# Kernel optimization log

Hardware: AMD Instinct MI355X
Metric: run time of the kernel (lower is better)

Reference implementation:

```python
import jax, jax.numpy as jnp
import numpy as np

N_NODES = 100_000
N_EDGES = 1_600_000
D_IN = 128
D_HID = 128
D_OUT = 128
N_GRAPHS = 1024


def setup_inputs() -> dict:
    key = jax.random.key(0)
    ks = jax.random.split(key, 7)
    x = jax.random.normal(ks[0], (N_NODES, D_IN), dtype=jnp.float32)
    edge_index = jax.random.randint(ks[1], (2, N_EDGES), 0, N_NODES, dtype=jnp.int32)
    batch = jnp.sort(jax.random.randint(ks[2], (N_NODES,), 0, N_GRAPHS, dtype=jnp.int32))
    W1 = jax.random.normal(ks[3], (D_IN, D_HID), dtype=jnp.float32) * (1.0 / np.sqrt(D_IN))
    b1 = jax.random.normal(ks[4], (D_HID,), dtype=jnp.float32) * 0.01
    W2 = jax.random.normal(ks[5], (D_HID, D_OUT), dtype=jnp.float32) * (1.0 / np.sqrt(D_HID))
    b2 = jax.random.normal(ks[6], (D_OUT,), dtype=jnp.float32) * 0.01
    return {"x": x, "edge_index": edge_index, "batch": batch,
            "W1": W1, "b1": b1, "W2": W2, "b2": b2, "num_graphs": N_GRAPHS}


def gcn_conv(x, edge_index, W, b):
    """PyG GCNConv: add self-loops, symmetric deg^{-1/2} norm, linear, scatter-add."""
    n = x.shape[0]
    xw = x @ W  # [N, H] -- transform before propagate, as PyG does
    loop = jnp.arange(n, dtype=edge_index.dtype)
    src = jnp.concatenate([edge_index[0], loop])  # message source (x_j)
    dst = jnp.concatenate([edge_index[1], loop])  # aggregation target
    deg = jax.ops.segment_sum(jnp.ones_like(dst, dtype=xw.dtype), dst, num_segments=n)
    dinv = jnp.where(deg > 0, jax.lax.rsqrt(deg), 0.0)
    norm = dinv[src] * dinv[dst]  # [E+N]
    out = jax.ops.segment_sum(norm[:, None] * xw[src], dst, num_segments=n)
    return out + b


def reference(x, edge_index, batch, W1, b1, W2, b2, num_graphs):
    h = jax.nn.relu(gcn_conv(x, edge_index, W1, b1))
    h = gcn_conv(h, edge_index, W2, b2)
    # global_mean_pool over graph ids
    s = jax.ops.segment_sum(h, batch, num_segments=num_graphs)          # [G, D_OUT]
    cnt = jax.ops.segment_sum(jnp.ones((x.shape[0],), h.dtype), batch, num_segments=num_graphs)
    return s / jnp.maximum(cnt, 1.0)[:, None]
```

## Files before the change

### kernel.cpp

```cpp
#include <hip/hip_runtime.h>

constexpr int D = 128;
constexpr int PAD = 48;
constexpr int EBLK = 4096;
constexpr int WNODE = 256;
constexpr int CAPW = 32;
constexpr int SCAP = 8192;

typedef __attribute__((ext_vector_type(8))) short short8;
typedef __attribute__((ext_vector_type(4))) float floatx4;
typedef __attribute__((ext_vector_type(2))) float floatx2;
typedef unsigned short ushort_t;
typedef unsigned char uchar_t;

static inline size_t ws_align(size_t x) { return (x + 255) & ~size_t(255); }

__device__ inline unsigned pack_bf16(float a, float b) {
  unsigned ua = __float_as_uint(a), ub = __float_as_uint(b);
  ua += 0x7fffu + ((ua >> 16) & 1u);
  ub += 0x7fffu + ((ub >> 16) & 1u);
  return ((ua >> 16) & 0xffffu) | (ub & 0xffff0000u);
}
__device__ inline ushort_t f32_to_bf16u(float f) {
  unsigned u = __float_as_uint(f);
  u += 0x7fffu + ((u >> 16) & 1u);
  return (ushort_t)(u >> 16);
}
__device__ inline float bf16u_to_f32(ushort_t u) {
  return __uint_as_float(((unsigned)u) << 16);
}
__device__ inline uchar_t f32_to_fp8(float v) {
  int p = __builtin_amdgcn_cvt_pk_fp8_f32(v, v, 0, false);
  return (uchar_t)(p & 0xff);
}
__device__ inline void fp8x4_acc(unsigned u, float* v) {
  floatx2 a = __builtin_amdgcn_cvt_pk_f32_fp8((int)u, false);
  floatx2 b = __builtin_amdgcn_cvt_pk_f32_fp8((int)u, true);
  v[0] += a.x; v[1] += a.y; v[2] += b.x; v[3] += b.y;
}
__device__ inline void fp8x4_acc2(unsigned u, floatx2* v) {
  v[0] += __builtin_amdgcn_cvt_pk_f32_fp8((int)u, false);
  v[1] += __builtin_amdgcn_cvt_pk_f32_fp8((int)u, true);
}

__global__ __launch_bounds__(256) void k_prep(
    const int* __restrict__ src, const int* __restrict__ dst, int E,
    int nstrips, int nw,
    unsigned* __restrict__ bucket, int* __restrict__ bkcnt,
    uint2* __restrict__ spill, int* __restrict__ scnt,
    const float* __restrict__ W1, const float* __restrict__ W2,
    ushort_t* __restrict__ w1t, ushort_t* __restrict__ w2t, int nbin) {
  const int b = blockIdx.x;
  const int t = threadIdx.x;
  if (b < nbin) {
    __shared__ int lcnt[512];
    for (int i = t; i < nw; i += 256) lcnt[i] = 0;
    __syncthreads();
    const int base = b * EBLK;
    const int end = min(base + EBLK, E);
    for (int j = base + t; j < end; j += 256) {
      int ss = src[j], dd = dst[j];
      int wnd = dd >> 8;
      unsigned pk = ((unsigned)(dd & 255) << 17) | (unsigned)ss;
      int p = atomicAdd(&lcnt[wnd], 1);
      if (p < CAPW) {
        bucket[((size_t)wnd * nstrips + b) * CAPW + p] = pk;
      } else {
        int sp = atomicAdd(scnt, 1);
        if (sp < SCAP) spill[sp] = make_uint2((unsigned)ss, (unsigned)dd);
      }
    }
    __syncthreads();
    for (int i = t; i < nw; i += 256)
      bkcnt[(size_t)i * nstrips + b] = min(lcnt[i], CAPW);
    return;
  }
  {
    int idx = (b - nbin) * 256 + t;
    int k = idx >> 7, n = idx & 127;
    w1t[n * 128 + k] = f32_to_bf16u(W1[idx]);
    w2t[n * 128 + k] = f32_to_bf16u(W2[idx]);
  }
}

__global__ __launch_bounds__(256) void k_fill(
    const unsigned* __restrict__ bucket, const int* __restrict__ bkcnt,
    const uint2* __restrict__ spill, const int* __restrict__ scnt,
    int* __restrict__ cnt, int* __restrict__ csrp, int N, int nstrips) {
  __shared__ int lc[WNODE];
  __shared__ int ls[WNODE * PAD];
  const int w = blockIdx.x;
  const int t = threadIdx.x;
  const int wbase = w << 8;
  const int nn = min(WNODE, N - wbase);
  for (int i = t; i < WNODE; i += 256) lc[i] = 0;
  __syncthreads();
  const int* bc = bkcnt + (size_t)w * nstrips;
  const unsigned* bwin = bucket + (size_t)w * nstrips * CAPW;
  const int wid = t >> 6, l = t & 63;
  const int sgrp = l >> 3;
  const int ui = l & 7;
  for (int sb0 = wid * 8; sb0 < nstrips; sb0 += 32) {
    int s = sb0 + sgrp;
    int c = (s < nstrips) ? bc[s] : 0;
    uint4 v = make_uint4(0u, 0u, 0u, 0u);
    if (ui * 4 < c)
      v = ((const uint4*)(bwin + (size_t)s * CAPW))[ui];
    unsigned e[4] = {v.x, v.y, v.z, v.w};
#pragma unroll
    for (int u = 0; u < 4; ++u) {
      int j = ui * 4 + u;
      if (j < c) {
        unsigned pk = e[u];
        int dl = (int)(pk >> 17);
        int p = atomicAdd(&lc[dl], 1);
        if (p < PAD) ls[dl * PAD + p] = (int)(pk & 0x1FFFFu);
      }
    }
  }
  {
    int ns = min(*scnt, SCAP);
    for (int j = t; j < ns; j += 256) {
      uint2 e = spill[j];
      if ((int)(e.y >> 8) == w) {
        int dl = (int)(e.y & 255u);
        int p = atomicAdd(&lc[dl], 1);
        if (p < PAD) ls[dl * PAD + p] = (int)e.x;
      }
    }
  }
  __syncthreads();
  const int total = nn * PAD;
  int4* dp = (int4*)(csrp + (size_t)wbase * PAD);
  const int4* sp = (const int4*)ls;
  for (int i = t; i < (total >> 2); i += 256) dp[i] = sp[i];
  for (int i = (total & ~3) + t; i < total; i += 256)
    csrp[(size_t)wbase * PAD + i] = ls[i];
  for (int i = t; i < nn; i += 256) cnt[wbase + i] = lc[i];
}

template <bool A_FP32>
__global__ __launch_bounds__(512) void k_gemm(
    const void* __restrict__ Av, const ushort_t* __restrict__ Wt,
    const int* __restrict__ cnt, uchar_t* __restrict__ Y, int N) {
  __shared__ ushort_t As[64 * 128];
  __shared__ ushort_t Bs[128 * 128];
  const int t = threadIdx.x;
  const int rowBase = blockIdx.x * 64;

  {
    const uint4* g = (const uint4*)Wt;
#pragma unroll
    for (int i = 0; i < 4; ++i) {
      int idx = t + 512 * i;
      int r = idx >> 4, c = idx & 15;
      int cs = c ^ (r & 15);
      *(uint4*)&Bs[r * 128 + cs * 8] = g[idx];
    }
  }
  if (A_FP32) {
    const float4* A = (const float4*)Av;
#pragma unroll
    for (int i = 0; i < 4; ++i) {
      int idx = t + 512 * i;
      int r = idx >> 5, c4 = idx & 31;
      int grow = rowBase + r;
      float4 v = make_float4(0.f, 0.f, 0.f, 0.f);
      if (grow < N) v = A[(size_t)grow * 32 + c4];
      int cs = (c4 >> 1) ^ (r & 15);
      unsigned* p = (unsigned*)&As[r * 128 + cs * 8 + (c4 & 1) * 4];
      p[0] = pack_bf16(v.x, v.y);
      p[1] = pack_bf16(v.z, v.w);
    }
  } else {
    const uint4* A = (const uint4*)Av;
#pragma unroll
    for (int i = 0; i < 2; ++i) {
      int idx = t + 512 * i;
      int r = idx >> 4, c = idx & 15;
      int grow = rowBase + r;
      uint4 v = make_uint4(0u, 0u, 0u, 0u);
      if (grow < N) v = A[(size_t)grow * 16 + c];
      int cs = c ^ (r & 15);
      *(uint4*)&As[r * 128 + cs * 8] = v;
    }
  }
  __syncthreads();

  const int w = t >> 6;
  const int l = t & 63;
  const int qd = l >> 4, lm = l & 15;
  const int mrow = (w >> 1) * 16;
  const int jb = (w & 1) * 4;

  floatx4 acc[4];
#pragma unroll
  for (int j = 0; j < 4; ++j) acc[j] = (floatx4){0.f, 0.f, 0.f, 0.f};

#pragma unroll
  for (int ks = 0; ks < 4; ++ks) {
    const int ch = ks * 4 + qd;
    const int chs = ch ^ lm;
    short8 a0 = *(const short8*)&As[(mrow + lm) * 128 + chs * 8];
#pragma unroll
    for (int j = 0; j < 4; ++j) {
      short8 b = *(const short8*)&Bs[((jb + j) * 16 + lm) * 128 + chs * 8];
      acc[j] = __builtin_amdgcn_mfma_f32_16x16x32_bf16(a0, b, acc[j], 0, 0, 0);
    }
  }

  float s[4];
#pragma unroll
  for (int r = 0; r < 4; ++r) {
    int grow = rowBase + mrow + qd * 4 + r;
    s[r] = (grow < N) ? rsqrtf(1.f + (float)cnt[grow]) : 0.f;
  }
#pragma unroll
  for (int j = 0; j < 4; ++j)
#pragma unroll
    for (int r = 0; r < 4; ++r) {
      int grow = rowBase + mrow + qd * 4 + r;
      if (grow < N)
        Y[(size_t)grow * 128 + (jb + j) * 16 + lm] = f32_to_fp8(s[r] * acc[j][r]);
    }
}

__global__ __launch_bounds__(512) void k_agg_gemm(
    const uchar_t* __restrict__ y, const int* __restrict__ csrp,
    const int* __restrict__ cnt, const float* __restrict__ bias,
    const ushort_t* __restrict__ Wt, uchar_t* __restrict__ Y2, int N) {
  __shared__ ushort_t Hs[16 * 128];
  __shared__ ushort_t Bs[128 * 128];
  const int t = threadIdx.x;
  const int wid = t >> 6;
  const int l = t & 63;
  const int eg = l >> 4, q = l & 15;
  const int base = blockIdx.x * 16;
  {
    const uint4* g = (const uint4*)Wt;
#pragma unroll
    for (int i = 0; i < 4; ++i) {
      int idx = t + 512 * i;
      int r = idx >> 4, c = idx & 15;
      int cs = c ^ (r & 15);
      *(uint4*)&Bs[r * 128 + cs * 8] = g[idx];
    }
  }
  const int n0 = base + wid * 2;
  if (n0 < N) {
    const int n1 = n0 + 1;
    const bool hasB = (n1 < N);
    const uint2* yb = (const uint2*)y;
    int degA0 = cnt[n0];
    int degB0 = hasB ? cnt[n1] : 0;
    float dvA = rsqrtf(1.f + (float)degA0);
    float dvB = rsqrtf(1.f + (float)degB0);
    int degA = degA0 > PAD ? PAD : degA0;
    int degB = degB0 > PAD ? PAD : degB0;
    int idxA = 0, idxB = 0;
    if (l < PAD) {
      idxA = csrp[(size_t)n0 * PAD + l];
      if (hasB) idxB = csrp[(size_t)n1 * PAD + l];
    }
    uint2 sv = make_uint2(0u, 0u);
    if (eg == 0) sv = yb[(size_t)n0 * 16 + q];
    else if (eg == 1 && hasB) sv = yb[(size_t)n1 * 16 + q];
    floatx2 vA[4], vB[4];
#pragma unroll
    for (int k = 0; k < 4; ++k) { vA[k] = (floatx2){0.f, 0.f}; vB[k] = (floatx2){0.f, 0.f}; }
    const int dmax = degA > degB ? degA : degB;
    const int iters = (dmax + 15) >> 4;
    for (int it = 0; it < iters; ++it) {
      int p0 = it * 16 + eg;
      int p1 = p0 + 4, p2 = p0 + 8, p3 = p0 + 12;
      int a0 = __shfl(idxA, p0);
      int a1 = __shfl(idxA, p1);
      int a2 = __shfl(idxA, p2);
      int a3 = __shfl(idxA, p3);
      int b0 = __shfl(idxB, p0);
      int b1 = __shfl(idxB, p1);
      int b2 = __shfl(idxB, p2);
      int b3 = __shfl(idxB, p3);
      if (p0 < degA) { uint2 v = yb[(size_t)a0 * 16 + q]; fp8x4_acc2(v.x, vA); fp8x4_acc2(v.y, vA + 2); }
      if (p0 < degB) { uint2 v = yb[(size_t)b0 * 16 + q]; fp8x4_acc2(v.x, vB); fp8x4_acc2(v.y, vB + 2); }
      if (p1 < degA) { uint2 v = yb[(size_t)a1 * 16 + q]; fp8x4_acc2(v.x, vA); fp8x4_acc2(v.y, vA + 2); }
      if (p1 < degB) { uint2 v = yb[(size_t)b1 * 16 + q]; fp8x4_acc2(v.x, vB); fp8x4_acc2(v.y, vB + 2); }
      if (p2 < degA) { uint2 v = yb[(size_t)a2 * 16 + q]; fp8x4_acc2(v.x, vA); fp8x4_acc2(v.y, vA + 2); }
      if (p2 < degB) { uint2 v = yb[(size_t)b2 * 16 + q]; fp8x4_acc2(v.x, vB); fp8x4_acc2(v.y, vB + 2); }
      if (p3 < degA) { uint2 v = yb[(size_t)a3 * 16 + q]; fp8x4_acc2(v.x, vA); fp8x4_acc2(v.y, vA + 2); }
      if (p3 < degB) { uint2 v = yb[(size_t)b3 * 16 + q]; fp8x4_acc2(v.x, vB); fp8x4_acc2(v.y, vB + 2); }
    }
    float fA[8] = {vA[0].x, vA[0].y, vA[1].x, vA[1].y, vA[2].x, vA[2].y, vA[3].x, vA[3].y};
    float fB[8] = {vB[0].x, vB[0].y, vB[1].x, vB[1].y, vB[2].x, vB[2].y, vB[3].x, vB[3].y};
#pragma unroll
    for (int k = 0; k < 8; ++k) {
      fA[k] += __shfl_xor(fA[k], 32); fA[k] += __shfl_xor(fA[k], 16);
      fB[k] += __shfl_xor(fB[k], 32); fB[k] += __shfl_xor(fB[k], 16);
    }
    if (eg == 0 || (eg == 1 && hasB)) {
      float dv = (eg == 0) ? dvA : dvB;
      float f[8];
#pragma unroll
      for (int k = 0; k < 8; ++k) f[k] = (eg == 0) ? fA[k] : fB[k];
      fp8x4_acc(sv.x, f); fp8x4_acc(sv.y, f + 4);
      float4 c0 = ((const float4*)bias)[2 * q];
      float4 c1 = ((const float4*)bias)[2 * q + 1];
      float o[8];
      o[0] = dv * f[0] + c0.x; o[1] = dv * f[1] + c0.y;
      o[2] = dv * f[2] + c0.z; o[3] = dv * f[3] + c0.w;
      o[4] = dv * f[4] + c1.x; o[5] = dv * f[5] + c1.y;
      o[6] = dv * f[6] + c1.z; o[7] = dv * f[7] + c1.w;
#pragma unroll
      for (int k = 0; k < 8; ++k) o[k] = fmaxf(o[k], 0.f);
      uint4 pk;
      pk.x = pack_bf16(o[0], o[1]); pk.y = pack_bf16(o[2], o[3]);
      pk.z = pack_bf16(o[4], o[5]); pk.w = pack_bf16(o[6], o[7]);
      int r = wid * 2 + eg;
      int cs = q ^ r;
      *(uint4*)&Hs[r * 128 + cs * 8] = pk;
    }
  }
  __syncthreads();
  floatx4 acc = (floatx4){0.f, 0.f, 0.f, 0.f};
#pragma unroll
  for (int ks = 0; ks < 4; ++ks) {
    const int ch = ks * 4 + eg;
    const int chs = ch ^ q;
    short8 a0 = *(const short8*)&Hs[q * 128 + chs * 8];
    short8 b = *(const short8*)&Bs[(wid * 16 + q) * 128 + chs * 8];
    acc = __builtin_amdgcn_mfma_f32_16x16x32_bf16(a0, b, acc, 0, 0, 0);
  }
  float s[4];
#pragma unroll
  for (int r = 0; r < 4; ++r) {
    int grow = base + eg * 4 + r;
    s[r] = (grow < N) ? rsqrtf(1.f + (float)cnt[grow]) : 0.f;
  }
#pragma unroll
  for (int r = 0; r < 4; ++r) {
    int grow = base + eg * 4 + r;
    if (grow < N)
      Y2[(size_t)grow * 128 + wid * 16 + q] = f32_to_fp8(s[r] * acc[r]);
  }
}

template <bool RELU>
__global__ __launch_bounds__(256) void k_aggregate(
    const uchar_t* __restrict__ y, const int* __restrict__ csrp,
    const int* __restrict__ cnt, const float* __restrict__ bias,
    ushort_t* __restrict__ out, int N) {
  const int wid = threadIdx.x >> 6;
  const int n0 = blockIdx.x * 8 + wid * 2;
  if (n0 >= N) return;
  const int n1 = n0 + 1;
  const bool hasB = (n1 < N);
  const int l = threadIdx.x & 63;
  const int eg = l >> 4, q = l & 15;
  const uint2* yb = (const uint2*)y;
  int degA0 = cnt[n0];
  int degB0 = hasB ? cnt[n1] : 0;
  float dvA = rsqrtf(1.f + (float)degA0);
  float dvB = rsqrtf(1.f + (float)degB0);
  int degA = degA0 > PAD ? PAD : degA0;
  int degB = degB0 > PAD ? PAD : degB0;
  int idxA = 0, idxB = 0;
  if (l < PAD) {
    idxA = csrp[(size_t)n0 * PAD + l];
    if (hasB) idxB = csrp[(size_t)n1 * PAD + l];
  }
  uint2 sv = make_uint2(0u, 0u);
  if (eg == 0) sv = yb[(size_t)n0 * 16 + q];
  else if (eg == 1 && hasB) sv = yb[(size_t)n1 * 16 + q];
  floatx2 vA[4], vB[4];
#pragma unroll
  for (int k = 0; k < 4; ++k) { vA[k] = (floatx2){0.f, 0.f}; vB[k] = (floatx2){0.f, 0.f}; }
  const int dmax = degA > degB ? degA : degB;
  const int iters = (dmax + 15) >> 4;
  for (int it = 0; it < iters; ++it) {
    int p0 = it * 16 + eg;
    int p1 = p0 + 4, p2 = p0 + 8, p3 = p0 + 12;
    int a0 = __shfl(idxA, p0);
    int a1 = __shfl(idxA, p1);
    int a2 = __shfl(idxA, p2);
    int a3 = __shfl(idxA, p3);
    int b0 = __shfl(idxB, p0);
    int b1 = __shfl(idxB, p1);
    int b2 = __shfl(idxB, p2);
    int b3 = __shfl(idxB, p3);
    if (p0 < degA) { uint2 v = yb[(size_t)a0 * 16 + q]; fp8x4_acc2(v.x, vA); fp8x4_acc2(v.y, vA + 2); }
    if (p0 < degB) { uint2 v = yb[(size_t)b0 * 16 + q]; fp8x4_acc2(v.x, vB); fp8x4_acc2(v.y, vB + 2); }
    if (p1 < degA) { uint2 v = yb[(size_t)a1 * 16 + q]; fp8x4_acc2(v.x, vA); fp8x4_acc2(v.y, vA + 2); }
    if (p1 < degB) { uint2 v = yb[(size_t)b1 * 16 + q]; fp8x4_acc2(v.x, vB); fp8x4_acc2(v.y, vB + 2); }
    if (p2 < degA) { uint2 v = yb[(size_t)a2 * 16 + q]; fp8x4_acc2(v.x, vA); fp8x4_acc2(v.y, vA + 2); }
    if (p2 < degB) { uint2 v = yb[(size_t)b2 * 16 + q]; fp8x4_acc2(v.x, vB); fp8x4_acc2(v.y, vB + 2); }
    if (p3 < degA) { uint2 v = yb[(size_t)a3 * 16 + q]; fp8x4_acc2(v.x, vA); fp8x4_acc2(v.y, vA + 2); }
    if (p3 < degB) { uint2 v = yb[(size_t)b3 * 16 + q]; fp8x4_acc2(v.x, vB); fp8x4_acc2(v.y, vB + 2); }
  }
  float fA[8] = {vA[0].x, vA[0].y, vA[1].x, vA[1].y, vA[2].x, vA[2].y, vA[3].x, vA[3].y};
  float fB[8] = {vB[0].x, vB[0].y, vB[1].x, vB[1].y, vB[2].x, vB[2].y, vB[3].x, vB[3].y};
#pragma unroll
  for (int k = 0; k < 8; ++k) {
    fA[k] += __shfl_xor(fA[k], 32); fA[k] += __shfl_xor(fA[k], 16);
    fB[k] += __shfl_xor(fB[k], 32); fB[k] += __shfl_xor(fB[k], 16);
  }
  if (eg == 0 || (eg == 1 && hasB)) {
    float dv = (eg == 0) ? dvA : dvB;
    int node = (eg == 0) ? n0 : n1;
    float f[8];
#pragma unroll
    for (int k = 0; k < 8; ++k) f[k] = (eg == 0) ? fA[k] : fB[k];
    fp8x4_acc(sv.x, f); fp8x4_acc(sv.y, f + 4);
    float4 c0 = ((const float4*)bias)[2 * q];
    float4 c1 = ((const float4*)bias)[2 * q + 1];
    float o[8];
    o[0] = dv * f[0] + c0.x; o[1] = dv * f[1] + c0.y;
    o[2] = dv * f[2] + c0.z; o[3] = dv * f[3] + c0.w;
    o[4] = dv * f[4] + c1.x; o[5] = dv * f[5] + c1.y;
    o[6] = dv * f[6] + c1.z; o[7] = dv * f[7] + c1.w;
    if (RELU) {
#pragma unroll
      for (int k = 0; k < 8; ++k) o[k] = fmaxf(o[k], 0.f);
    }
    uint4 pk;
    pk.x = pack_bf16(o[0], o[1]); pk.y = pack_bf16(o[2], o[3]);
    pk.z = pack_bf16(o[4], o[5]); pk.w = pack_bf16(o[6], o[7]);
    ((uint4*)out)[(size_t)node * 16 + q] = pk;
  }
}

__global__ __launch_bounds__(512) void k_pool(
    const ushort_t* __restrict__ h, const int* __restrict__ batch,
    float* __restrict__ out, int N, int G) {
  __shared__ float part[4][128];
  int g = blockIdx.x;
  int col = threadIdx.x & 127;
  int pr = threadIdx.x >> 7;
  int lo = 0, hi = N;
  while (lo < hi) { int m = (lo + hi) >> 1; if (batch[m] < g) lo = m + 1; else hi = m; }
  int start = lo;
  hi = N;
  while (lo < hi) { int m = (lo + hi) >> 1; if (batch[m] <= g) lo = m + 1; else hi = m; }
  int end = lo;
  float sum = 0.f;
  for (int r = start + pr; r < end; r += 4) sum += bf16u_to_f32(h[(size_t)r * D + col]);
  part[pr][col] = sum;
  __syncthreads();
  if (pr == 0) {
    float s = part[0][col] + part[1][col] + part[2][col] + part[3][col];
    int c = end - start;
    out[(size_t)g * D + col] = s / (float)(c > 0 ? c : 1);
  }
}

extern "C" void kernel_launch(void* const* d_in, const int* in_sizes, int n_in,
                              void* d_out, int out_size, void* d_ws, size_t ws_size,
                              hipStream_t stream) {
  const float* x  = (const float*)d_in[0];
  const int* edge = (const int*)d_in[1];
  const int* batch = (const int*)d_in[2];
  const float* W1 = (const float*)d_in[3];
  const float* b1 = (const float*)d_in[4];
  const float* W2 = (const float*)d_in[5];
  const float* b2 = (const float*)d_in[6];
  float* out = (float*)d_out;

  const int N = in_sizes[0] / D;
  const int E = in_sizes[1] / 2;
  const int G = out_size / D;
  const int* esrc = edge;
  const int* edst = edge + E;

  const int nstrips = (E + EBLK - 1) / EBLK;
  const int nw = (N + WNODE - 1) / WNODE;

  char* ws = (char*)d_ws;
  size_t off = 0;
  auto alloc = [&](size_t bytes) {
    char* p = ws + off;
    off = ws_align(off + bytes);
    return p;
  };
  uchar_t* bufY = (uchar_t*)alloc((size_t)N * D);
  uchar_t* bufY2 = (uchar_t*)alloc((size_t)N * D);
  ushort_t* bufH = (ushort_t*)alloc((size_t)N * D * 2);
  int* cnt = (int*)alloc((size_t)N * 4);
  int* csrp = (int*)alloc((size_t)N * PAD * 4);
  ushort_t* w1t = (ushort_t*)alloc((size_t)D * D * 2);
  ushort_t* w2t = (ushort_t*)alloc((size_t)D * D * 2);
  unsigned* bucket = (unsigned*)alloc((size_t)nw * nstrips * CAPW * 4);
  int* bkcnt = (int*)alloc((size_t)nw * nstrips * 4);
  uint2* spill = (uint2*)alloc((size_t)SCAP * 8);
  int* scnt = (int*)alloc(256);

  const int tb = 256;

  hipMemsetAsync(scnt, 0, 4, stream);

  const int nbin = nstrips;
  const int nwp = (D * D) / 256;
  k_prep<<<nbin + nwp, tb, 0, stream>>>(esrc, edst, E, nstrips, nw,
                                        bucket, bkcnt, spill, scnt,
                                        W1, W2, w1t, w2t, nbin);

  k_fill<<<nw, tb, 0, stream>>>(bucket, bkcnt, spill, scnt, cnt, csrp, N, nstrips);

  const int gblk = (N + 63) / 64;
  k_gemm<true><<<gblk, 512, 0, stream>>>(x, w1t, cnt, bufY, N);
  const int fblk = (N + 15) / 16;
  k_agg_gemm<<<fblk, 512, 0, stream>>>(bufY, csrp, cnt, b1, w2t, bufY2, N);
  const int ablk = (N + 7) / 8;
  k_aggregate<false><<<ablk, 256, 0, stream>>>(bufY2, csrp, cnt, b2, bufH, N);
  k_pool<<<G, 512, 0, stream>>>(bufH, batch, out, N, G);
}
```

Baseline: 264.7 us.

## Process 64 nodes per fused aggregate-GEMM block to amortize weight staging

The fused layer-1 aggregation plus layer-2 GEMM kernel now handles 64 rows per block instead of 16. It does this by looping four aggregation passes, then running a 64x128 MFMA tile in which each wave computes four 16x16 output tiles. This spreads the 32KB W2 load into LDS over four times as many nodes and cuts the grid size by four. In exchange it uses more LDS (Hs grows to 16KB), which may lower occupancy, and each block runs its gather passes serially before a single sync.

```diff
diff --git a/kernel.cpp b/kernel.cpp
--- a/kernel.cpp
+++ b/kernel.cpp
@@ -229,13 +229,13 @@
     const uchar_t* __restrict__ y, const int* __restrict__ csrp,
     const int* __restrict__ cnt, const float* __restrict__ bias,
     const ushort_t* __restrict__ Wt, uchar_t* __restrict__ Y2, int N) {
-  __shared__ ushort_t Hs[16 * 128];
+  __shared__ ushort_t Hs[64 * 128];
   __shared__ ushort_t Bs[128 * 128];
   const int t = threadIdx.x;
   const int wid = t >> 6;
   const int l = t & 63;
   const int eg = l >> 4, q = l & 15;
-  const int base = blockIdx.x * 16;
+  const int base = blockIdx.x * 64;
   {
     const uint4* g = (const uint4*)Wt;
 #pragma unroll
@@ -246,102 +246,115 @@
       *(uint4*)&Bs[r * 128 + cs * 8] = g[idx];
     }
   }
-  const int n0 = base + wid * 2;
-  if (n0 < N) {
-    const int n1 = n0 + 1;
-    const bool hasB = (n1 < N);
-    const uint2* yb = (const uint2*)y;
-    int degA0 = cnt[n0];
-    int degB0 = hasB ? cnt[n1] : 0;
-    float dvA = rsqrtf(1.f + (float)degA0);
-    float dvB = rsqrtf(1.f + (float)degB0);
-    int degA = degA0 > PAD ? PAD : degA0;
-    int degB = degB0 > PAD ? PAD : degB0;
-    int idxA = 0, idxB = 0;
-    if (l < PAD) {
-      idxA = csrp[(size_t)n0 * PAD + l];
-      if (hasB) idxB = csrp[(size_t)n1 * PAD + l];
-    }
-    uint2 sv = make_uint2(0u, 0u);
-    if (eg == 0) sv = yb[(size_t)n0 * 16 + q];
-    else if (eg == 1 && hasB) sv = yb[(size_t)n1 * 16 + q];
-    floatx2 vA[4], vB[4];
-#pragma unroll
-    for (int k = 0; k < 4; ++k) { vA[k] = (floatx2){0.f, 0.f}; vB[k] = (floatx2){0.f, 0.f}; }
-    const int dmax = degA > degB ? degA : degB;
-    const int iters = (dmax + 15) >> 4;
-    for (int it = 0; it < iters; ++it) {
-      int p0 = it * 16 + eg;
-      int p1 = p0 + 4, p2 = p0 + 8, p3 = p0 + 12;
-      int a0 = __shfl(idxA, p0);
-      int a1 = __shfl(idxA, p1);
-      int a2 = __shfl(idxA, p2);
-      int a3 = __shfl(idxA, p3);
-      int b0 = __shfl(idxB, p0);
-      int b1 = __shfl(idxB, p1);
-      int b2 = __shfl(idxB, p2);
-      int b3 = __shfl(idxB, p3);
-      if (p0 < degA) { uint2 v = yb[(size_t)a0 * 16 + q]; fp8x4_acc2(v.x, vA); fp8x4_acc2(v.y, vA + 2); }
-      if (p0 < degB) { uint2 v = yb[(size_t)b0 * 16 + q]; fp8x4_acc2(v.x, vB); fp8x4_acc2(v.y, vB + 2); }
-      if (p1 < degA) { uint2 v = yb[(size_t)a1 * 16 + q]; fp8x4_acc2(v.x, vA); fp8x4_acc2(v.y, vA + 2); }
-      if (p1 < degB) { uint2 v = yb[(size_t)b1 * 16 + q]; fp8x4_acc2(v.x, vB); fp8x4_acc2(v.y, vB + 2); }
-      if (p2 < degA) { uint2 v = yb[(size_t)a2 * 16 + q]; fp8x4_acc2(v.x, vA); fp8x4_acc2(v.y, vA + 2); }
-      if (p2 < degB) { uint2 v = yb[(size_t)b2 * 16 + q]; fp8x4_acc2(v.x, vB); fp8x4_acc2(v.y, vB + 2); }
-      if (p3 < degA) { uint2 v = yb[(size_t)a3 * 16 + q]; fp8x4_acc2(v.x, vA); fp8x4_acc2(v.y, vA + 2); }
-      if (p3 < degB) { uint2 v = yb[(size_t)b3 * 16 + q]; fp8x4_acc2(v.x, vB); fp8x4_acc2(v.y, vB + 2); }
-    }
-    float fA[8] = {vA[0].x, vA[0].y, vA[1].x, vA[1].y, vA[2].x, vA[2].y, vA[3].x, vA[3].y};
-    float fB[8] = {vB[0].x, vB[0].y, vB[1].x, vB[1].y, vB[2].x, vB[2].y, vB[3].x, vB[3].y};
-#pragma unroll
-    for (int k = 0; k < 8; ++k) {
-      fA[k] += __shfl_xor(fA[k], 32); fA[k] += __shfl_xor(fA[k], 16);
-      fB[k] += __shfl_xor(fB[k], 32); fB[k] += __shfl_xor(fB[k], 16);
-    }
-    if (eg == 0 || (eg == 1 && hasB)) {
-      float dv = (eg == 0) ? dvA : dvB;
-      float f[8];
-#pragma unroll
-      for (int k = 0; k < 8; ++k) f[k] = (eg == 0) ? fA[k] : fB[k];
-      fp8x4_acc(sv.x, f); fp8x4_acc(sv.y, f + 4);
-      float4 c0 = ((const float4*)bias)[2 * q];
-      float4 c1 = ((const float4*)bias)[2 * q + 1];
-      float o[8];
-      o[0] = dv * f[0] + c0.x; o[1] = dv * f[1] + c0.y;
-      o[2] = dv * f[2] + c0.z; o[3] = dv * f[3] + c0.w;
-      o[4] = dv * f[4] + c1.x; o[5] = dv * f[5] + c1.y;
-      o[6] = dv * f[6] + c1.z; o[7] = dv * f[7] + c1.w;
-#pragma unroll
-      for (int k = 0; k < 8; ++k) o[k] = fmaxf(o[k], 0.f);
-      uint4 pk;
-      pk.x = pack_bf16(o[0], o[1]); pk.y = pack_bf16(o[2], o[3]);
-      pk.z = pack_bf16(o[4], o[5]); pk.w = pack_bf16(o[6], o[7]);
-      int r = wid * 2 + eg;
-      int cs = q ^ r;
-      *(uint4*)&Hs[r * 128 + cs * 8] = pk;
+  const uint2* yb = (const uint2*)y;
+#pragma unroll 1
+  for (int pass = 0; pass < 4; ++pass) {
+    const int n0 = base + pass * 16 + wid * 2;
+    if (n0 < N) {
+      const int n1 = n0 + 1;
+      const bool hasB = (n1 < N);
+      int degA0 = cnt[n0];
+      int degB0 = hasB ? cnt[n1] : 0;
+      float dvA = rsqrtf(1.f + (float)degA0);
+      float dvB = rsqrtf(1.f + (float)degB0);
+      int degA = degA0 > PAD ? PAD : degA0;
+      int degB = degB0 > PAD ? PAD : degB0;
+      int idxA = 0, idxB = 0;
+      if (l < PAD) {
+        idxA = csrp[(size_t)n0 * PAD + l];
+        if (hasB) idxB = csrp[(size_t)n1 * PAD + l];
+      }
+      uint2 sv = make_uint2(0u, 0u);
+      if (eg == 0) sv = yb[(size_t)n0 * 16 + q];
+      else if (eg == 1 && hasB) sv = yb[(size_t)n1 * 16 + q];
+      floatx2 vA[4], vB[4];
+#pragma unroll
+      for (int k = 0; k < 4; ++k) { vA[k] = (floatx2){0.f, 0.f}; vB[k] = (floatx2){0.f, 0.f}; }
+      const int dmax = degA > degB ? degA : degB;
+      const int iters = (dmax + 15) >> 4;
+      for (int it = 0; it < iters; ++it) {
+        int p0 = it * 16 + eg;
+        int p1 = p0 + 4, p2 = p0 + 8, p3 = p0 + 12;
+        int a0 = __shfl(idxA, p0);
+        int a1 = __shfl(idxA, p1);
+        int a2 = __shfl(idxA, p2);
+        int a3 = __shfl(idxA, p3);
+        int b0 = __shfl(idxB, p0);
+        int b1 = __shfl(idxB, p1);
+        int b2 = __shfl(idxB, p2);
+        int b3 = __shfl(idxB, p3);
+        if (p0 < degA) { uint2 v = yb[(size_t)a0 * 16 + q]; fp8x4_acc2(v.x, vA); fp8x4_acc2(v.y, vA + 2); }
+        if (p0 < degB) { uint2 v = yb[(size_t)b0 * 16 + q]; fp8x4_acc2(v.x, vB); fp8x4_acc2(v.y, vB + 2); }
+        if (p1 < degA) { uint2 v = yb[(size_t)a1 * 16 + q]; fp8x4_acc2(v.x, vA); fp8x4_acc2(v.y, vA + 2); }
+        if (p1 < degB) { uint2 v = yb[(size_t)b1 * 16 + q]; fp8x4_acc2(v.x, vB); fp8x4_acc2(v.y, vB + 2); }
+        if (p2 < degA) { uint2 v = yb[(size_t)a2 * 16 + q]; fp8x4_acc2(v.x, vA); fp8x4_acc2(v.y, vA + 2); }
+        if (p2 < degB) { uint2 v = yb[(size_t)b2 * 16 + q]; fp8x4_acc2(v.x, vB); fp8x4_acc2(v.y, vB + 2); }
+        if (p3 < degA) { uint2 v = yb[(size_t)a3 * 16 + q]; fp8x4_acc2(v.x, vA); fp8x4_acc2(v.y, vA + 2); }
+        if (p3 < degB) { uint2 v = yb[(size_t)b3 * 16 + q]; fp8x4_acc2(v.x, vB); fp8x4_acc2(v.y, vB + 2); }
+      }
+      float fA[8] = {vA[0].x, vA[0].y, vA[1].x, vA[1].y, vA[2].x, vA[2].y, vA[3].x, vA[3].y};
+      float fB[8] = {vB[0].x, vB[0].y, vB[1].x, vB[1].y, vB[2].x, vB[2].y, vB[3].x, vB[3].y};
+#pragma unroll
+      for (int k = 0; k < 8; ++k) {
+        fA[k] += __shfl_xor(fA[k], 32); fA[k] += __shfl_xor(fA[k], 16);
+        fB[k] += __shfl_xor(fB[k], 32); fB[k] += __shfl_xor(fB[k], 16);
+      }
+      if (eg == 0 || (eg == 1 && hasB)) {
+        float dv = (eg == 0) ? dvA : dvB;
+        float f[8];
+#pragma unroll
+        for (int k = 0; k < 8; ++k) f[k] = (eg == 0) ? fA[k] : fB[k];
+        fp8x4_acc(sv.x, f); fp8x4_acc(sv.y, f + 4);
+        float4 c0 = ((const float4*)bias)[2 * q];
+        float4 c1 = ((const float4*)bias)[2 * q + 1];
+        float o[8];
+        o[0] = dv * f[0] + c0.x; o[1] = dv * f[1] + c0.y;
+        o[2] = dv * f[2] + c0.z; o[3] = dv * f[3] + c0.w;
+        o[4] = dv * f[4] + c1.x; o[5] = dv * f[5] + c1.y;
+        o[6] = dv * f[6] + c1.z; o[7] = dv * f[7] + c1.w;
+#pragma unroll
+        for (int k = 0; k < 8; ++k) o[k] = fmaxf(o[k], 0.f);
+        uint4 pk;
+        pk.x = pack_bf16(o[0], o[1]); pk.y = pack_bf16(o[2], o[3]);
+        pk.z = pack_bf16(o[4], o[5]); pk.w = pack_bf16(o[6], o[7]);
+        int r = pass * 16 + wid * 2 + eg;
+        int cs = q ^ (r & 15);
+        *(uint4*)&Hs[r * 128 + cs * 8] = pk;
+      }
     }
   }
   __syncthreads();
-  floatx4 acc = (floatx4){0.f, 0.f, 0.f, 0.f};
+  const int qd = eg, lm = q;
+  const int mrow = (wid >> 1) * 16;
+  const int jb = (wid & 1) * 4;
+  floatx4 acc[4];
+#pragma unroll
+  for (int j = 0; j < 4; ++j) acc[j] = (floatx4){0.f, 0.f, 0.f, 0.f};
 #pragma unroll
   for (int ks = 0; ks < 4; ++ks) {
-    const int ch = ks * 4 + eg;
-    const int chs = ch ^ q;
-    short8 a0 = *(const short8*)&Hs[q * 128 + chs * 8];
-    short8 b = *(const short8*)&Bs[(wid * 16 + q) * 128 + chs * 8];
-    acc = __builtin_amdgcn_mfma_f32_16x16x32_bf16(a0, b, acc, 0, 0, 0);
+    const int ch = ks * 4 + qd;
+    const int chs = ch ^ lm;
+    short8 a0 = *(const short8*)&Hs[(mrow + lm) * 128 + chs * 8];
+#pragma unroll
+    for (int j = 0; j < 4; ++j) {
+      short8 b = *(const short8*)&Bs[((jb + j) * 16 + lm) * 128 + chs * 8];
+      acc[j] = __builtin_amdgcn_mfma_f32_16x16x32_bf16(a0, b, acc[j], 0, 0, 0);
+    }
   }
   float s[4];
 #pragma unroll
   for (int r = 0; r < 4; ++r) {
-    int grow = base + eg * 4 + r;
+    int grow = base + mrow + qd * 4 + r;
     s[r] = (grow < N) ? rsqrtf(1.f + (float)cnt[grow]) : 0.f;
   }
 #pragma unroll
-  for (int r = 0; r < 4; ++r) {
-    int grow = base + eg * 4 + r;
-    if (grow < N)
-      Y2[(size_t)grow * 128 + wid * 16 + q] = f32_to_fp8(s[r] * acc[r]);
-  }
+  for (int j = 0; j < 4; ++j)
+#pragma unroll
+    for (int r = 0; r < 4; ++r) {
+      int grow = base + mrow + qd * 4 + r;
+      if (grow < N)
+        Y2[(size_t)grow * 128 + (jb + j) * 16 + lm] = f32_to_fp8(s[r] * acc[j][r]);
+    }
 }
 
 template <bool RELU>
@@ -506,8 +519,7 @@
 
   const int gblk = (N + 63) / 64;
   k_gemm<true><<<gblk, 512, 0, stream>>>(x, w1t, cnt, bufY, N);
-  const int fblk = (N + 15) / 16;
-  k_agg_gemm<<<fblk, 512, 0, stream>>>(bufY, csrp, cnt, b1, w2t, bufY2, N);
+  k_agg_gemm<<<gblk, 512, 0, stream>>>(bufY, csrp, cnt, b1, w2t, bufY2, N);
   const int ablk = (N + 7) / 8;
   k_aggregate<false><<<ablk, 256, 0, stream>>>(bufY2, csrp, cnt, b2, bufH, N);
   k_pool<<<G, 512, 0, stream>>>(bufH, batch, out, N, G);
```

Measured after the change: 277.2 us. 1.05x slower.
